# Optimization experiments

Measured on AMD Instinct MI355X. Metric: run time of the kernel, lower is better.

## Reference

```python
import jax, jax.numpy as jnp
import numpy as np
from jax import lax

COS_BASIS_NO = 24
SCALE = 6.0
SHIFT = 1.0


def make_kern_basis(T_no):
    # [24, T_no] raised-cosine log-time basis, matching the torch loop exactly
    i = jnp.arange(COS_BASIS_NO, dtype=jnp.float32)
    phi = (jnp.pi / 2.0) * i                                  # [24]
    x = jnp.arange(T_no, dtype=jnp.float32)
    raw = SCALE * jnp.log(x + SHIFT + 1e-7)                   # [T_no]
    basis = 0.5 * jnp.cos(raw[None, :] - phi[:, None]) + 0.5  # [24, T_no]
    inside = (raw[None, :] >= phi[:, None] - jnp.pi) & (raw[None, :] <= phi[:, None] + jnp.pi)
    return jnp.where(inside, basis, 0.0)


def causal_grouped_conv(x, kern, sub_no, T_no):
    # x: [B, sub_no, T], kern: [sub_no*hid, T_no] (already flipped like torch)
    # left-pad T_no-1 zeros == the torch zero-padded buffer; cross-correlation
    rhs = kern[:, None, :]  # OIH with I=1 per group
    return lax.conv_general_dilated(
        x, rhs, window_strides=(1,), padding=[(T_no - 1, 0)],
        feature_group_count=sub_no,
        dimension_numbers=("NCH", "OIH", "NCH"))


def setup_inputs() -> dict:
    key = jax.random.key(0)
    ks = jax.random.split(key, 10)
    B, T_data = 8, 5000
    sub_no, E_no, I_no, T_no, hid_no = 20, 2000, 200, 400, 16
    inp = {
        "S_e": jax.random.uniform(ks[0], (B, T_data, E_no), dtype=jnp.float32),
        "S_i": jax.random.uniform(ks[1], (B, T_data, I_no), dtype=jnp.float32),
        "E_scale": jnp.zeros((E_no,), jnp.float32),
        "I_scale": jnp.zeros((I_no,), jnp.float32),
        "W_e_layer1": jax.random.normal(ks[2], (sub_no * hid_no, COS_BASIS_NO), jnp.float32) * 0.01,
        "W_i_layer1": jax.random.normal(ks[3], (sub_no * hid_no, COS_BASIS_NO), jnp.float32) * 0.01,
        "W_layer2": jnp.full((sub_no, hid_no), -1.0, jnp.float32),
        "b_layer1": jnp.zeros((sub_no * hid_no,), jnp.float32),
        "C_syn_e_raw": jax.random.normal(ks[4], (sub_no, E_no), jnp.float32) * 0.01,
        "C_syn_i_raw": jax.random.normal(ks[5], (sub_no, I_no), jnp.float32) * 0.01,
        "V_o": jnp.zeros((1,), jnp.float32),
        "temp": jnp.asarray(1.0, jnp.float32),
        "T_no": T_no,
        "test": 1,
    }
    return inp


def reference(S_e, S_i, E_scale, I_scale, W_e_layer1, W_i_layer1, W_layer2,
              b_layer1, C_syn_e_raw, C_syn_i_raw, V_o, temp, T_no, test):
    sub_no = C_syn_e_raw.shape[0]
    hid_no = W_layer2.shape[1]
    B, T_data, _ = S_e.shape

    if test:
        C_syn_e = jax.nn.softmax(C_syn_e_raw / temp, axis=0)
        C_syn_i = jax.nn.softmax(C_syn_i_raw / temp, axis=0)
    else:
        eps = 1e-8
        ku, kv = jax.random.split(jax.random.key(42))
        u_e = jax.random.uniform(ku, C_syn_e_raw.shape, dtype=C_syn_e_raw.dtype)
        u_i = jax.random.uniform(kv, C_syn_i_raw.shape, dtype=C_syn_i_raw.dtype)
        g_e = -jnp.log(-jnp.log(u_e + eps) + eps)
        g_i = -jnp.log(-jnp.log(u_i + eps) + eps)
        C_syn_e = jax.nn.softmax((C_syn_e_raw + g_e) / temp, axis=0)
        C_syn_i = jax.nn.softmax((C_syn_i_raw + g_i) / temp, axis=0)

    # scale synapses and project onto subunits: [B,T,E] x [E,sub] -> [B,T,sub]
    syn_e = jnp.einsum("bte,se->bts", S_e * jnp.exp(E_scale)[None, None, :], C_syn_e)
    syn_i = jnp.einsum("bti,si->bts", S_i * jnp.exp(I_scale)[None, None, :], C_syn_i)

    kern_basis = make_kern_basis(T_no)                        # [24, T_no]
    ke = jnp.flip(W_e_layer1 @ kern_basis, axis=1)            # [sub*hid, T_no]
    ki = jnp.flip(W_i_layer1 @ kern_basis, axis=1)

    xe = jnp.transpose(syn_e, (0, 2, 1))                      # [B, sub, T]
    xi = jnp.transpose(syn_i, (0, 2, 1))
    conv_e = causal_grouped_conv(xe, ke, sub_no, T_no)        # [B, sub*hid, T]
    conv_i = causal_grouped_conv(xi, ki, sub_no, T_no)
    layer1 = jnp.tanh(conv_e + conv_i + b_layer1[None, :, None])

    # grouped 1x1 conv == per-subunit weighted reduction over hid
    h = layer1.reshape(B, sub_no, hid_no, T_data)
    sub_out = jnp.einsum("bshT,sh->bTs", h, jnp.exp(W_layer2))  # [B, T, sub]
    final = jnp.sum(sub_out, axis=-1) + V_o                    # [B, T]
    return final, sub_out, C_syn_e, C_syn_i
```

## Files before the change

### kernel.cpp

```cpp
#include <hip/hip_runtime.h>
#include <math.h>

#define PI_F 3.14159265358979323846f
#define BSTRIDE 404

__global__ __launch_bounds__(256) void prep_kernel(
    const float* __restrict__ Ce_raw, const float* __restrict__ Ci_raw,
    const float* __restrict__ Escale, const float* __restrict__ Iscale,
    const float* __restrict__ temp,
    float* __restrict__ CsT_e, float* __restrict__ CsT_i,
    float* __restrict__ basis,
    float* __restrict__ outCe, float* __restrict__ outCi)
{
    int id = blockIdx.x * 256 + threadIdx.x;
    if (id < 2000) {
        int e = id;
        float t = temp[0];
        float v[20];
        float m = -1e30f;
        #pragma unroll
        for (int s = 0; s < 20; ++s) { v[s] = Ce_raw[s * 2000 + e] / t; m = fmaxf(m, v[s]); }
        float sum = 0.f;
        #pragma unroll
        for (int s = 0; s < 20; ++s) { v[s] = expf(v[s] - m); sum += v[s]; }
        float inv = 1.f / sum;
        float sc = expf(Escale[e]);
        #pragma unroll
        for (int s = 0; s < 20; ++s) {
            float p = v[s] * inv;
            outCe[s * 2000 + e] = p;
            CsT_e[e * 20 + s] = p * sc;
        }
    } else if (id < 2200) {
        int e = id - 2000;
        float t = temp[0];
        float v[20];
        float m = -1e30f;
        #pragma unroll
        for (int s = 0; s < 20; ++s) { v[s] = Ci_raw[s * 200 + e] / t; m = fmaxf(m, v[s]); }
        float sum = 0.f;
        #pragma unroll
        for (int s = 0; s < 20; ++s) { v[s] = expf(v[s] - m); sum += v[s]; }
        float inv = 1.f / sum;
        float sc = expf(Iscale[e]);
        #pragma unroll
        for (int s = 0; s < 20; ++s) {
            float p = v[s] * inv;
            outCi[s * 200 + e] = p;
            CsT_i[e * 20 + s] = p * sc;
        }
    } else if (id < 2200 + 24 * BSTRIDE) {
        int idx = id - 2200;
        int j = idx / BSTRIDE, d = idx - j * BSTRIDE;
        float val = 0.f;
        if (d < 400) {
            float raw = 6.0f * logf((float)d + 1.0f + 1e-7f);
            float ph = (PI_F * 0.5f) * (float)j;
            if (raw >= ph - PI_F && raw <= ph + PI_F) val = 0.5f * cosf(raw - ph) + 0.5f;
        }
        basis[idx] = val;
    } else if (id < 11896 + 48) {
        int row = 2000 + (id - 11896);
        #pragma unroll
        for (int s = 0; s < 20; ++s) CsT_e[row * 20 + s] = 0.f;
    } else if (id < 11944 + 56) {
        int row = 200 + (id - 11944);
        #pragma unroll
        for (int s = 0; s < 20; ++s) CsT_i[row * 20 + s] = 0.f;
    }
}

template <int NCHUNK>
__global__ __launch_bounds__(256) void syn_kernel(
    const float* __restrict__ S, const float* __restrict__ CsT,
    float* __restrict__ syn, int Eno)
{
    __shared__ float4 tile[64 * 33];
    float* red = reinterpret_cast<float*>(tile);
    const int tid = threadIdx.x;
    const int lane = tid & 63;
    const int w = __builtin_amdgcn_readfirstlane(tid >> 6);
    const int r0 = blockIdx.x * 64;

    float acc[20];
    #pragma unroll
    for (int s = 0; s < 20; ++s) acc[s] = 0.f;

    for (int ch = 0; ch < NCHUNK; ++ch) {
        const int ebase = ch * 128;
        #pragma unroll
        for (int i = 0; i < 8; ++i) {
            int f = tid + i * 256;
            int row = f >> 5, col4 = f & 31;
            int e0 = ebase + col4 * 4;
            float4 v = make_float4(0.f, 0.f, 0.f, 0.f);
            if (e0 + 4 <= Eno)
                v = *reinterpret_cast<const float4*>(S + (size_t)(r0 + row) * Eno + e0);
            tile[row * 33 + col4] = v;
        }
        __syncthreads();

        const float4* crow = reinterpret_cast<const float4*>(CsT + (size_t)(ebase + w * 32) * 20);
        #pragma unroll
        for (int c4 = 0; c4 < 8; ++c4) {
            float4 v = tile[lane * 33 + w * 8 + c4];
            const float4* ct = crow + c4 * 20;
            float vv[4] = {v.x, v.y, v.z, v.w};
            #pragma unroll
            for (int q = 0; q < 4; ++q) {
                float sv = vv[q];
                #pragma unroll
                for (int c5 = 0; c5 < 5; ++c5) {
                    float4 cc = ct[q * 5 + c5];
                    acc[c5 * 4 + 0] = fmaf(sv, cc.x, acc[c5 * 4 + 0]);
                    acc[c5 * 4 + 1] = fmaf(sv, cc.y, acc[c5 * 4 + 1]);
                    acc[c5 * 4 + 2] = fmaf(sv, cc.z, acc[c5 * 4 + 2]);
                    acc[c5 * 4 + 3] = fmaf(sv, cc.w, acc[c5 * 4 + 3]);
                }
            }
        }
        __syncthreads();
    }

    #pragma unroll
    for (int s = 0; s < 20; ++s) red[(lane * 4 + w) * 20 + s] = acc[s];
    __syncthreads();

    #pragma unroll
    for (int i = 0; i < 5; ++i) {
        int p = tid + i * 256;
        int row = p & 63, s = p >> 6;
        float a = red[(row * 4 + 0) * 20 + s] + red[(row * 4 + 1) * 20 + s]
                + red[(row * 4 + 2) * 20 + s] + red[(row * 4 + 3) * 20 + s];
        int r = r0 + row;
        int b = r / 5000, t = r - b * 5000;
        syn[((size_t)b * 20 + s) * 5000 + t] = a;
    }
}

__device__ const int CJ_LO[24] = {0,0,0,0,0,0,0,0,0,4,4,8,12,16,20,28,36,48,64,84,108,140,184,240};
__device__ const int CJ_NB[24] = {1,1,1,1,2,2,3,3,4,4,5,6,7,9,12,15,19,25,31,41,53,65,54,40};

__device__ __forceinline__ int phys4(int g) {
    return (g & ~15) | ((g >> 1) & 7) | ((g & 1) << 3);
}

__global__ __launch_bounds__(128) void conv_kernel(
    const float* __restrict__ syn_e, const float* __restrict__ syn_i,
    const float* __restrict__ basis,
    const float* __restrict__ W_e, const float* __restrict__ W_i,
    const float* __restrict__ b1, const float* __restrict__ W2,
    float* __restrict__ sub_out)
{
    __shared__ float4 win4[464];
    float2* win2 = reinterpret_cast<float2*>(win4);
    const int tid = threadIdx.x;
    const int tile = blockIdx.x, s = blockIdx.y, bz = blockIdx.z;
    const int t0 = tile * 512;

    const float* se = syn_e + ((size_t)bz * 20 + s) * 5000;
    const float* si = syn_i + ((size_t)bz * 20 + s) * 5000;
    for (int l = tid; l < 920; l += 128) {
        int t = t0 - 404 + l;
        float ve = 0.f, vi = 0.f;
        if ((unsigned)t < 5000u) { ve = se[t]; vi = si[t]; }
        int g = l >> 1;
        win2[2 * phys4(g) + (l & 1)] = make_float2(ve, vi);
    }
    __syncthreads();

    float z[16][4];
    #pragma unroll
    for (int h = 0; h < 16; ++h) {
        float bv = b1[s * 16 + h];
        #pragma unroll
        for (int k = 0; k < 4; ++k) z[h][k] = bv;
    }

    const int base = 4 * tid + 400;

    for (int j = 0; j < 24; ++j) {
        const float* bj = basis + j * BSTRIDE;
        const int lo = CJ_LO[j];
        const int nb = CJ_NB[j];
        float be0 = 0.f, be1 = 0.f, be2 = 0.f, be3 = 0.f;
        float bi0 = 0.f, bi1 = 0.f, bi2 = 0.f, bi3 = 0.f;

        auto body = [&](const float4& V0, const float4& V1,
                        const float4& V2, const float4& V3, int dd0) {
            float c0 = bj[dd0], c1 = bj[dd0 + 1], c2 = bj[dd0 + 2], c3 = bj[dd0 + 3];
            be0 = fmaf(c0, V2.x, be0); bi0 = fmaf(c0, V2.y, bi0);
            be1 = fmaf(c0, V2.z, be1); bi1 = fmaf(c0, V2.w, bi1);
            be2 = fmaf(c0, V3.x, be2); bi2 = fmaf(c0, V3.y, bi2);
            be3 = fmaf(c0, V3.z, be3); bi3 = fmaf(c0, V3.w, bi3);
            be0 = fmaf(c1, V1.z, be0); bi0 = fmaf(c1, V1.w, bi0);
            be1 = fmaf(c1, V2.x, be1); bi1 = fmaf(c1, V2.y, bi1);
            be2 = fmaf(c1, V2.z, be2); bi2 = fmaf(c1, V2.w, bi2);
            be3 = fmaf(c1, V3.x, be3); bi3 = fmaf(c1, V3.y, bi3);
            be0 = fmaf(c2, V1.x, be0); bi0 = fmaf(c2, V1.y, bi0);
            be1 = fmaf(c2, V1.z, be1); bi1 = fmaf(c2, V1.w, bi1);
            be2 = fmaf(c2, V2.x, be2); bi2 = fmaf(c2, V2.y, bi2);
            be3 = fmaf(c2, V2.z, be3); bi3 = fmaf(c2, V2.w, bi3);
            be0 = fmaf(c3, V0.z, be0); bi0 = fmaf(c3, V0.w, bi0);
            be1 = fmaf(c3, V1.x, be1); bi1 = fmaf(c3, V1.y, bi1);
            be2 = fmaf(c3, V1.z, be2); bi2 = fmaf(c3, V1.w, bi2);
            be3 = fmaf(c3, V2.x, be3); bi3 = fmaf(c3, V2.y, bi3);
        };

        int g = (base - lo) >> 1;
        int pa = phys4(g);
        int pb = phys4(g + 2);
        float4 a0 = win4[pa], a1 = win4[pa + 8];
        float4 b0 = win4[pb], b1v = win4[pb + 8];

        int d0 = lo;
        int bb = 0;
        for (; bb + 2 <= nb; bb += 2) {
            body(a0, a1, b0, b1v, d0);
            int pn = phys4(g - 2);
            b0 = win4[pn]; b1v = win4[pn + 8];
            body(b0, b1v, a0, a1, d0 + 4);
            pn = phys4(g - 4);
            a0 = win4[pn]; a1 = win4[pn + 8];
            g -= 4;
            d0 += 8;
        }
        if (bb < nb)
            body(a0, a1, b0, b1v, d0);

        #pragma unroll
        for (int h = 0; h < 16; ++h) {
            float we = W_e[(s * 16 + h) * 24 + j];
            float wi = W_i[(s * 16 + h) * 24 + j];
            z[h][0] = fmaf(we, be0, fmaf(wi, bi0, z[h][0]));
            z[h][1] = fmaf(we, be1, fmaf(wi, bi1, z[h][1]));
            z[h][2] = fmaf(we, be2, fmaf(wi, bi2, z[h][2]));
            z[h][3] = fmaf(we, be3, fmaf(wi, bi3, z[h][3]));
        }
    }

    float w2v[16];
    #pragma unroll
    for (int h = 0; h < 16; ++h) w2v[h] = __expf(W2[s * 16 + h]);

    #pragma unroll
    for (int k = 0; k < 4; ++k) {
        int t = t0 + 4 * tid + k;
        if (t < 5000) {
            float acc = 0.f;
            #pragma unroll
            for (int h = 0; h < 16; ++h) {
                float e2 = __expf(2.0f * z[h][k]);
                float th = 1.0f - 2.0f / (e2 + 1.0f);
                acc = fmaf(w2v[h], th, acc);
            }
            sub_out[((size_t)bz * 5000 + t) * 20 + s] = acc;
        }
    }
}

__global__ __launch_bounds__(256) void final_kernel(
    const float* __restrict__ sub_out, const float* __restrict__ V_o,
    float* __restrict__ fin)
{
    int r = blockIdx.x * 256 + threadIdx.x;
    if (r < 40000) {
        const float* p = sub_out + (size_t)r * 20;
        float a = V_o[0];
        #pragma unroll
        for (int s = 0; s < 20; ++s) a += p[s];
        fin[r] = a;
    }
}

extern "C" void kernel_launch(void* const* d_in, const int* in_sizes, int n_in,
                              void* d_out, int out_size, void* d_ws, size_t ws_size,
                              hipStream_t stream)
{
    const float* S_e     = (const float*)d_in[0];
    const float* S_i     = (const float*)d_in[1];
    const float* E_scale = (const float*)d_in[2];
    const float* I_scale = (const float*)d_in[3];
    const float* W_e     = (const float*)d_in[4];
    const float* W_i     = (const float*)d_in[5];
    const float* W2      = (const float*)d_in[6];
    const float* b1      = (const float*)d_in[7];
    const float* Ce_raw  = (const float*)d_in[8];
    const float* Ci_raw  = (const float*)d_in[9];
    const float* V_o     = (const float*)d_in[10];
    const float* temp    = (const float*)d_in[11];

    float* out     = (float*)d_out;
    float* fin     = out;
    float* sub_out = out + 40000;
    float* outCe   = out + 840000;
    float* outCi   = out + 880000;

    float* ws    = (float*)d_ws;
    float* CsT_e = ws;
    float* CsT_i = ws + 40960;
    float* basis = ws + 46080;
    float* syn_e = ws + 55776;
    float* syn_i = ws + 855776;

    prep_kernel<<<47, 256, 0, stream>>>(Ce_raw, Ci_raw, E_scale, I_scale, temp,
                                        CsT_e, CsT_i, basis, outCe, outCi);
    syn_kernel<16><<<625, 256, 0, stream>>>(S_e, CsT_e, syn_e, 2000);
    syn_kernel<2><<<625, 256, 0, stream>>>(S_i, CsT_i, syn_i, 200);
    conv_kernel<<<dim3(10, 20, 8), 128, 0, stream>>>(syn_e, syn_i, basis,
                                                     W_e, W_i, b1, W2, sub_out);
    final_kernel<<<157, 256, 0, stream>>>(sub_out, V_o, fin);
}
```

Baseline: 289.1 us.

## Double-buffer syn tile loads and software-pipeline conv basis loop

The synapse projection kernel now prefetches the next input chunk into registers while computing on the current shared-memory buffer. This removes one barrier per chunk and hides global load latency. The conv kernel's inner loop is unrolled by eight with window and basis loads issued one to three steps ahead, and basis coefficients are read as float4. The cost is higher register pressure and more LDS use, which could lower occupancy. A guard pad added in front of the window lets the look-ahead loads read slightly before the start.

```diff
diff --git a/kernel.cpp b/kernel.cpp
--- a/kernel.cpp
+++ b/kernel.cpp
@@ -75,7 +75,7 @@
     const float* __restrict__ S, const float* __restrict__ CsT,
     float* __restrict__ syn, int Eno)
 {
-    __shared__ float4 tile[64 * 33];
+    __shared__ float4 tile[2][64 * 33];
     float* red = reinterpret_cast<float*>(tile);
     const int tid = threadIdx.x;
     const int lane = tid & 63;
@@ -86,24 +86,43 @@
     #pragma unroll
     for (int s = 0; s < 20; ++s) acc[s] = 0.f;
 
-    for (int ch = 0; ch < NCHUNK; ++ch) {
+    float4 st[8];
+    auto issue = [&](int ch, float4 (&v)[8]) {
         const int ebase = ch * 128;
         #pragma unroll
         for (int i = 0; i < 8; ++i) {
             int f = tid + i * 256;
             int row = f >> 5, col4 = f & 31;
             int e0 = ebase + col4 * 4;
-            float4 v = make_float4(0.f, 0.f, 0.f, 0.f);
+            v[i] = make_float4(0.f, 0.f, 0.f, 0.f);
             if (e0 + 4 <= Eno)
-                v = *reinterpret_cast<const float4*>(S + (size_t)(r0 + row) * Eno + e0);
-            tile[row * 33 + col4] = v;
-        }
+                v[i] = *reinterpret_cast<const float4*>(S + (size_t)(r0 + row) * Eno + e0);
+        }
+    };
+    auto put = [&](int buf, float4 (&v)[8]) {
+        #pragma unroll
+        for (int i = 0; i < 8; ++i) {
+            int f = tid + i * 256;
+            int row = f >> 5, col4 = f & 31;
+            tile[buf][row * 33 + col4] = v[i];
+        }
+    };
+
+    issue(0, st);
+    put(0, st);
+    int cur = 0;
+
+    for (int ch = 0; ch < NCHUNK; ++ch) {
+        float4 nx[8];
+        if (ch + 1 < NCHUNK) issue(ch + 1, nx);
         __syncthreads();
 
+        const int ebase = ch * 128;
         const float4* crow = reinterpret_cast<const float4*>(CsT + (size_t)(ebase + w * 32) * 20);
+        const float4* tl = tile[cur];
         #pragma unroll
         for (int c4 = 0; c4 < 8; ++c4) {
-            float4 v = tile[lane * 33 + w * 8 + c4];
+            float4 v = tl[lane * 33 + w * 8 + c4];
             const float4* ct = crow + c4 * 20;
             float vv[4] = {v.x, v.y, v.z, v.w};
             #pragma unroll
@@ -119,8 +138,10 @@
                 }
             }
         }
-        __syncthreads();
-    }
+        if (ch + 1 < NCHUNK) put(cur ^ 1, nx);
+        cur ^= 1;
+    }
+    __syncthreads();
 
     #pragma unroll
     for (int s = 0; s < 20; ++s) red[(lane * 4 + w) * 20 + s] = acc[s];
@@ -152,8 +173,9 @@
     const float* __restrict__ b1, const float* __restrict__ W2,
     float* __restrict__ sub_out)
 {
-    __shared__ float4 win4[464];
-    float2* win2 = reinterpret_cast<float2*>(win4);
+    __shared__ float4 win4[16 + 464];
+    float4* wbase = win4 + 16;
+    float2* win2 = reinterpret_cast<float2*>(wbase);
     const int tid = threadIdx.x;
     const int tile = blockIdx.x, s = blockIdx.y, bz = blockIdx.z;
     const int t0 = tile * 512;
@@ -180,53 +202,76 @@
     const int base = 4 * tid + 400;
 
     for (int j = 0; j < 24; ++j) {
-        const float* bj = basis + j * BSTRIDE;
+        const float4* bj4 = reinterpret_cast<const float4*>(basis + j * BSTRIDE);
         const int lo = CJ_LO[j];
         const int nb = CJ_NB[j];
+        const int co = lo >> 2;
         float be0 = 0.f, be1 = 0.f, be2 = 0.f, be3 = 0.f;
         float bi0 = 0.f, bi1 = 0.f, bi2 = 0.f, bi3 = 0.f;
 
         auto body = [&](const float4& V0, const float4& V1,
-                        const float4& V2, const float4& V3, int dd0) {
-            float c0 = bj[dd0], c1 = bj[dd0 + 1], c2 = bj[dd0 + 2], c3 = bj[dd0 + 3];
-            be0 = fmaf(c0, V2.x, be0); bi0 = fmaf(c0, V2.y, bi0);
-            be1 = fmaf(c0, V2.z, be1); bi1 = fmaf(c0, V2.w, bi1);
-            be2 = fmaf(c0, V3.x, be2); bi2 = fmaf(c0, V3.y, bi2);
-            be3 = fmaf(c0, V3.z, be3); bi3 = fmaf(c0, V3.w, bi3);
-            be0 = fmaf(c1, V1.z, be0); bi0 = fmaf(c1, V1.w, bi0);
-            be1 = fmaf(c1, V2.x, be1); bi1 = fmaf(c1, V2.y, bi1);
-            be2 = fmaf(c1, V2.z, be2); bi2 = fmaf(c1, V2.w, bi2);
-            be3 = fmaf(c1, V3.x, be3); bi3 = fmaf(c1, V3.y, bi3);
-            be0 = fmaf(c2, V1.x, be0); bi0 = fmaf(c2, V1.y, bi0);
-            be1 = fmaf(c2, V1.z, be1); bi1 = fmaf(c2, V1.w, bi1);
-            be2 = fmaf(c2, V2.x, be2); bi2 = fmaf(c2, V2.y, bi2);
-            be3 = fmaf(c2, V2.z, be3); bi3 = fmaf(c2, V2.w, bi3);
-            be0 = fmaf(c3, V0.z, be0); bi0 = fmaf(c3, V0.w, bi0);
-            be1 = fmaf(c3, V1.x, be1); bi1 = fmaf(c3, V1.y, bi1);
-            be2 = fmaf(c3, V1.z, be2); bi2 = fmaf(c3, V1.w, bi2);
-            be3 = fmaf(c3, V2.x, be3); bi3 = fmaf(c3, V2.y, bi3);
+                        const float4& V2, const float4& V3, const float4& c) {
+            be0 = fmaf(c.x, V2.x, be0); bi0 = fmaf(c.x, V2.y, bi0);
+            be1 = fmaf(c.x, V2.z, be1); bi1 = fmaf(c.x, V2.w, bi1);
+            be2 = fmaf(c.x, V3.x, be2); bi2 = fmaf(c.x, V3.y, bi2);
+            be3 = fmaf(c.x, V3.z, be3); bi3 = fmaf(c.x, V3.w, bi3);
+            be0 = fmaf(c.y, V1.z, be0); bi0 = fmaf(c.y, V1.w, bi0);
+            be1 = fmaf(c.y, V2.x, be1); bi1 = fmaf(c.y, V2.y, bi1);
+            be2 = fmaf(c.y, V2.z, be2); bi2 = fmaf(c.y, V2.w, bi2);
+            be3 = fmaf(c.y, V3.x, be3); bi3 = fmaf(c.y, V3.y, bi3);
+            be0 = fmaf(c.z, V1.x, be0); bi0 = fmaf(c.z, V1.y, bi0);
+            be1 = fmaf(c.z, V1.z, be1); bi1 = fmaf(c.z, V1.w, bi1);
+            be2 = fmaf(c.z, V2.x, be2); bi2 = fmaf(c.z, V2.y, bi2);
+            be3 = fmaf(c.z, V2.z, be3); bi3 = fmaf(c.z, V2.w, bi3);
+            be0 = fmaf(c.w, V0.z, be0); bi0 = fmaf(c.w, V0.w, bi0);
+            be1 = fmaf(c.w, V1.x, be1); bi1 = fmaf(c.w, V1.y, bi1);
+            be2 = fmaf(c.w, V1.z, be2); bi2 = fmaf(c.w, V1.w, bi2);
+            be3 = fmaf(c.w, V2.x, be3); bi3 = fmaf(c.w, V2.y, bi3);
         };
 
-        int g = (base - lo) >> 1;
-        int pa = phys4(g);
-        int pb = phys4(g + 2);
-        float4 a0 = win4[pa], a1 = win4[pa + 8];
-        float4 b0 = win4[pb], b1v = win4[pb + 8];
-
-        int d0 = lo;
+        const int g0 = (base - lo) >> 1;
+        auto LP = [&](int n, float4& lo4, float4& hi4) {
+            int p = phys4(g0 - 2 * n);
+            lo4 = wbase[p]; hi4 = wbase[p + 8];
+        };
+
+        float4 A0, A1, B0, B1, C0, C1, D0, D1;
+        float4 E0, E1, F0, F1, G0, G1, H0, H1;
+        LP(-1, A0, A1); LP(0, B0, B1); LP(1, C0, C1); LP(2, D0, D1);
+        float4 cB = bj4[co], cC = bj4[co + 1], cD = bj4[co + 2];
+
         int bb = 0;
-        for (; bb + 2 <= nb; bb += 2) {
-            body(a0, a1, b0, b1v, d0);
-            int pn = phys4(g - 2);
-            b0 = win4[pn]; b1v = win4[pn + 8];
-            body(b0, b1v, a0, a1, d0 + 4);
-            pn = phys4(g - 4);
-            a0 = win4[pn]; a1 = win4[pn + 8];
-            g -= 4;
-            d0 += 8;
-        }
-        if (bb < nb)
-            body(a0, a1, b0, b1v, d0);
+        while (bb + 8 <= nb) {
+            LP(bb + 3, E0, E1); float4 cE = bj4[co + bb + 3];
+            body(B0, B1, A0, A1, cB);
+            LP(bb + 4, F0, F1); float4 cF = bj4[co + bb + 4];
+            body(C0, C1, B0, B1, cC);
+            LP(bb + 5, G0, G1); float4 cG = bj4[co + bb + 5];
+            body(D0, D1, C0, C1, cD);
+            LP(bb + 6, H0, H1); float4 cH = bj4[co + bb + 6];
+            body(E0, E1, D0, D1, cE);
+            LP(bb + 7, A0, A1); float4 cI = bj4[co + bb + 7];
+            body(F0, F1, E0, E1, cF);
+            LP(bb + 8, B0, B1); cB = bj4[co + bb + 8];
+            body(G0, G1, F0, F1, cG);
+            LP(bb + 9, C0, C1); cC = bj4[co + bb + 9];
+            body(H0, H1, G0, G1, cH);
+            LP(bb + 10, D0, D1); cD = bj4[co + bb + 10];
+            body(A0, A1, H0, H1, cI);
+            bb += 8;
+        }
+        int r = nb - bb;
+        if (r > 0) { body(B0, B1, A0, A1, cB);
+          if (r > 1) { body(C0, C1, B0, B1, cC);
+            if (r > 2) { body(D0, D1, C0, C1, cD);
+              if (r > 3) { LP(bb + 3, E0, E1); float4 cE = bj4[co + bb + 3];
+                body(E0, E1, D0, D1, cE);
+                if (r > 4) { LP(bb + 4, F0, F1); float4 cF = bj4[co + bb + 4];
+                  body(F0, F1, E0, E1, cF);
+                  if (r > 5) { LP(bb + 5, G0, G1); float4 cG = bj4[co + bb + 5];
+                    body(G0, G1, F0, F1, cG);
+                    if (r > 6) { LP(bb + 6, H0, H1); float4 cH = bj4[co + bb + 6];
+                      body(H0, H1, G0, G1, cH); } } } } } } }
 
         #pragma unroll
         for (int h = 0; h < 16; ++h) {
```

Result: slower. 378.5 us (+30.9%).
